# Kernel tuning notes

Measured on AMD Instinct MI355X. Metric: run time of the kernel, lower is better.

## Reference

```python
import jax, jax.numpy as jnp
import numpy as np

N = 4_000_000   # points at level d
SIDE = 1024     # coordinate range per axis
HALF = SIDE // 2  # parent coord range


def setup_inputs() -> dict:
    key = jax.random.key(0)
    k1, k2 = jax.random.split(key)
    xyz = jax.random.randint(k1, (N, 3), 0, SIDE, dtype=jnp.int32)
    b = (jnp.arange(N, dtype=jnp.int32) % 4)[:, None]  # 4 batches
    coords = jnp.concatenate([b, xyz], axis=1)          # (N,4): [b,x,y,z]
    kernel = jnp.ones((8,), dtype=jnp.float32)          # frozen all-ones 2x2x2 conv weights
    return {"coords": coords, "kernel": kernel}


def _fog(coords, kernel):
    # pos(): occupancy code 2**(x%2 + 2*y%2 + 4*z%2)
    bits = coords[:, 1:4] & 1                       # (N,3)
    off = bits[:, 0] + 2 * bits[:, 1] + 4 * bits[:, 2]  # (N,) child offset in 2x2x2 window
    pos = jnp.exp2(off.astype(jnp.float32))         # (N,) code in {1,2,4,...,128}
    contrib = pos * kernel[off]                     # per-offset conv weight (all ones)
    # stride-2 conv: parent voxel = floor(xyz/2); linearize (b,z,y,x) into a key
    parent = coords[:, 1:4] >> 1                    # (N,3)
    keys = (((coords[:, 0].astype(jnp.int64) * HALF + parent[:, 2]) * HALF
             + parent[:, 1]) * HALF + parent[:, 0])
    ukeys, inv = jnp.unique(keys, return_inverse=True, size=N, fill_value=-1)
    feats = jax.ops.segment_sum(contrib, inv, num_segments=N)[:, None]  # (N,1)
    # decode padded unique keys back to coords; pad slots -> -1
    px = (ukeys % HALF).astype(jnp.int32)
    py = ((ukeys // HALF) % HALF).astype(jnp.int32)
    pz = ((ukeys // (HALF * HALF)) % HALF).astype(jnp.int32)
    pb = (ukeys // (HALF * HALF * HALF)).astype(jnp.int32)
    valid = (ukeys >= 0)[:, None]
    coords_out = jnp.where(valid, jnp.stack([pb, px, py, pz], axis=1), -1)
    return coords_out, feats


def reference(coords, kernel):
    return _fog(coords, kernel)
```

## Files before the change

### kernel.cpp

```cpp
#include <hip/hip_runtime.h>
#include <stdint.h>

typedef unsigned int u32;
typedef unsigned long long u64;

#define LBITS  14
#define LMASK  ((1u << LBITS) - 1u)
#define NBUCK  (1u << (29 - LBITS))
#define BWORDS (1u << (LBITS - 5))
#define WPL    (BWORDS / 64)
#define WOPAD  (BWORDS + BWORDS / 32)
#define FCAP   192
#define BPB    4
#define TILE_A 4096
#define RPT    (TILE_A / 256)
#define S2     4
#define CAP2   4608
#define RPT2   (CAP2 / 256)
#define RECV   4
#define CAP    224
#define SCAN_ELEM 2048

__device__ __forceinline__ u32 woidx(u32 w) { return w + (w >> 5); }

__device__ __forceinline__ void wsync() {
    asm volatile("s_waitcnt lgkmcnt(0)" ::: "memory");
}

__device__ __forceinline__ u32 make_key(int4 c) {
    return ((((u32)c.x * 512u + ((u32)c.w >> 1)) * 512u + ((u32)c.z >> 1)) * 512u)
           + ((u32)c.y >> 1);
}

__global__ void __launch_bounds__(256) phase_a(const int4* __restrict__ coords,
        u32* __restrict__ linrec, u32* __restrict__ histmat, int n, u32 NT) {
    __shared__ u32 h[4 * 256];
    u32 t = threadIdx.x, wave = t >> 6;
    for (u32 j = t; j < 1024u; j += 256u) h[j] = 0u;
    __syncthreads();
    u32 base = blockIdx.x * TILE_A;
    u32 m = min((u32)TILE_A, (u32)n - base);
    for (u32 j = t; j < m; j += 256u) {
        int4 c = coords[base + j];
        u32 key = make_key(c);
        u32 off = ((u32)c.y & 1u) | (((u32)c.z & 1u) << 1) | (((u32)c.w & 1u) << 2);
        u32 rec = (key << 3) | off;
        linrec[base + j] = rec;
        atomicAdd(&h[wave * 256u + (rec >> 24)], 1u);
    }
    __syncthreads();
    histmat[t * NT + blockIdx.x] = h[t] + h[256u + t] + h[512u + t] + h[768u + t];
}

__global__ void scan_reduce(const u32* __restrict__ data, u32* __restrict__ partial, u32 G) {
    __shared__ u32 s[256];
    u32 t = threadIdx.x;
    u32 base = blockIdx.x * SCAN_ELEM + t * 8u;
    u32 sum = 0;
    #pragma unroll
    for (int j = 0; j < 8; ++j) { u32 idx = base + j; if (idx < G) sum += data[idx]; }
    s[t] = sum; __syncthreads();
    for (int d = 128; d > 0; d >>= 1) { if ((int)t < d) s[t] += s[t + d]; __syncthreads(); }
    if (t == 0) partial[blockIdx.x] = s[0];
}

__global__ void scan_apply2(const u32* __restrict__ data, u32* __restrict__ out,
                            const u32* __restrict__ partial, u32 G, u32 NB,
                            u32* __restrict__ total) {
    __shared__ u32 s[256];
    __shared__ u32 pb[2];
    u32 t = threadIdx.x;
    u32 p = (t < NB) ? partial[t] : 0u;
    u32 pbef = (t < blockIdx.x) ? p : 0u;
    s[t] = pbef; __syncthreads();
    for (int d = 128; d > 0; d >>= 1) { if ((int)t < d) s[t] += s[t + d]; __syncthreads(); }
    if (t == 0) pb[0] = s[0];
    __syncthreads();
    if (total) {
        s[t] = p; __syncthreads();
        for (int d = 128; d > 0; d >>= 1) { if ((int)t < d) s[t] += s[t + d]; __syncthreads(); }
        if (t == 0) pb[1] = s[0];
        __syncthreads();
        if (blockIdx.x == NB - 1u && t == 0u) total[0] = pb[1];
    }
    u32 base = blockIdx.x * SCAN_ELEM + t * 8u;
    u32 v[8]; u32 sum = 0;
    #pragma unroll
    for (int j = 0; j < 8; ++j) {
        u32 idx = base + j;
        v[j] = (idx < G) ? data[idx] : 0u;
        sum += v[j];
    }
    s[t] = sum; __syncthreads();
    for (int d = 1; d < 256; d <<= 1) {
        u32 add = (t >= (u32)d) ? s[t - d] : 0u;
        __syncthreads(); s[t] += add; __syncthreads();
    }
    u32 run = s[t] - sum + pb[0];
    #pragma unroll
    for (int j = 0; j < 8; ++j) {
        u32 idx = base + j;
        if (idx < G) { u32 x = v[j]; out[idx] = run; run += x; }
    }
}

__global__ void __launch_bounds__(256) part1(const u32* __restrict__ linrec,
        const u32* __restrict__ histmat, u32* __restrict__ tmp,
        u32* __restrict__ cursor, int n, u32 NT) {
    __shared__ u32 stage[TILE_A];
    __shared__ u32 lcur[256];
    __shared__ u32 gb[256];
    __shared__ u32 wtot[4];
    u32 t = threadIdx.x, wave = t >> 6, lane = t & 63u;
    if (blockIdx.x < 128u) cursor[blockIdx.x * 256u + t] = 0u;
    u32 base = blockIdx.x * TILE_A;
    u32 m = min((u32)TILE_A, (u32)n - base);
    u32 m4 = m >> 2, rem = m & 3u;
    lcur[t] = 0u;
    __syncthreads();
    u32 recv[RPT]; u32 tailrec = 0u;
    const uint4* lr4 = (const uint4*)(linrec + base);
    #pragma unroll
    for (int k = 0; k < RPT / 4; ++k) {
        u32 j4 = (u32)k * 256u + t;
        if (j4 < m4) {
            uint4 v = lr4[j4];
            recv[k * 4 + 0] = v.x; recv[k * 4 + 1] = v.y;
            recv[k * 4 + 2] = v.z; recv[k * 4 + 3] = v.w;
            atomicAdd(&lcur[v.x >> 24], 1u);
            atomicAdd(&lcur[v.y >> 24], 1u);
            atomicAdd(&lcur[v.z >> 24], 1u);
            atomicAdd(&lcur[v.w >> 24], 1u);
        }
    }
    if (t < rem) {
        tailrec = linrec[base + (m & ~3u) + t];
        atomicAdd(&lcur[tailrec >> 24], 1u);
    }
    __syncthreads();
    u32 v = lcur[t];
    u32 incl = v;
    #pragma unroll
    for (int d = 1; d < 64; d <<= 1) {
        u32 x = __shfl_up(incl, d);
        if ((int)lane >= d) incl += x;
    }
    if (lane == 63u) wtot[wave] = incl;
    __syncthreads();
    u32 off = (wave > 0u ? wtot[0] : 0u) + (wave > 1u ? wtot[1] : 0u)
            + (wave > 2u ? wtot[2] : 0u);
    u32 excl = off + incl - v;
    lcur[t] = excl;
    gb[t] = histmat[t * NT + blockIdx.x] - excl;
    __syncthreads();
    #pragma unroll
    for (int k = 0; k < RPT / 4; ++k) {
        u32 j4 = (u32)k * 256u + t;
        if (j4 < m4) {
            #pragma unroll
            for (int e = 0; e < 4; ++e) {
                u32 rec = recv[k * 4 + e];
                u32 pos = atomicAdd(&lcur[rec >> 24], 1u);
                stage[pos] = rec;
            }
        }
    }
    if (t < rem) {
        u32 pos = atomicAdd(&lcur[tailrec >> 24], 1u);
        stage[pos] = tailrec;
    }
    __syncthreads();
    for (u32 j = t; j < m; j += 256u) {
        u32 rec = stage[j];
        tmp[gb[rec >> 24] + j] = rec;
    }
}

__global__ void __launch_bounds__(256) part2(const u32* __restrict__ tmp,
        const u32* __restrict__ histmat, u32* __restrict__ cursor,
        u32* __restrict__ buckrec, int n, u32 NT) {
    __shared__ u32 stage[CAP2];
    __shared__ u32 lcur[128];
    __shared__ u32 dstb[128];
    __shared__ u32 wtot[2];
    u32 t = threadIdx.x, lane = t & 63u;
    u32 c = blockIdx.x / S2, s = blockIdx.x % S2;
    u32 cs = histmat[c * NT];
    u32 ce = (c == 255u) ? (u32)n : histmat[(c + 1u) * NT];
    u32 L = ce - cs;
    u32 lo = cs + L * s / S2, hi = cs + L * (s + 1u) / S2;
    u32 cnt = hi - lo;
    if (cnt <= (u32)CAP2) {
        if (t < 128u) lcur[t] = 0u;
        __syncthreads();
        u32 recv[RPT2];
        #pragma unroll
        for (int k = 0; k < RPT2; ++k) {
            u32 j = (u32)k * 256u + t;
            if (j < cnt) {
                u32 rec = tmp[lo + j];
                recv[k] = rec;
                atomicAdd(&lcur[(rec >> 17) & 127u], 1u);
            }
        }
        __syncthreads();
        u32 v = 0, incl = 0;
        if (t < 128u) {
            v = lcur[t];
            incl = v;
            #pragma unroll
            for (int d = 1; d < 64; d <<= 1) {
                u32 x = __shfl_up(incl, d);
                if ((int)lane >= d) incl += x;
            }
            if (lane == 63u) wtot[t >> 6] = incl;
        }
        __syncthreads();
        if (t < 128u) {
            u32 off = (t >= 64u) ? wtot[0] : 0u;
            u32 excl = off + incl - v;
            u32 bucket = (c << 7) | t;
            u32 gbase = atomicAdd(&cursor[bucket], v);
            lcur[t] = excl;
            dstb[t] = bucket * (u32)CAP + gbase - excl;
        }
        __syncthreads();
        #pragma unroll
        for (int k = 0; k < RPT2; ++k) {
            u32 j = (u32)k * 256u + t;
            if (j < cnt) {
                u32 rec = recv[k];
                u32 pos = atomicAdd(&lcur[(rec >> 17) & 127u], 1u);
                stage[pos] = rec;
            }
        }
        __syncthreads();
        for (u32 j = t; j < cnt; j += 256u) {
            u32 rec = stage[j];
            buckrec[dstb[(rec >> 17) & 127u] + j] = rec;
        }
    } else {
        for (u32 i = lo + t; i < hi; i += 256u) {
            u32 rec = tmp[i];
            u32 b = rec >> 17;
            u32 pos = atomicAdd(&cursor[b], 1u);
            buckrec[b * (u32)CAP + pos] = rec;
        }
    }
}

__global__ void __launch_bounds__(256) pass_count(const u32* __restrict__ buckrec,
        const u32* __restrict__ bcnt, u32* __restrict__ ucount, int n) {
    __shared__ u32 bm[BPB][WOPAD];
    u32 wave = threadIdx.x >> 6, lane = threadIdx.x & 63u;
    u32 bucket = blockIdx.x * BPB + wave;
    u32* B = bm[wave];
    #pragma unroll
    for (int j = 0; j < WPL; ++j) B[woidx(lane * WPL + j)] = 0u;
    wsync();
    u32 start = bucket * (u32)CAP;
    u32 end = start + bcnt[bucket];
    for (u32 i = start + lane; i < end; i += 64u) {
        u32 lk = (buckrec[i] >> 3) & LMASK;
        atomicOr(&B[woidx(lk >> 5)], 1u << (lk & 31u));
    }
    wsync();
    u32 sum = 0;
    #pragma unroll
    for (int j = 0; j < WPL; ++j) sum += __popc(B[woidx(lane * WPL + j)]);
    #pragma unroll
    for (int d = 1; d < 64; d <<= 1) sum += __shfl_xor(sum, d);
    if (lane == 0u) ucount[bucket] = sum;
}

__global__ void __launch_bounds__(256) pass_emit(const u32* __restrict__ buckrec,
        const u32* __restrict__ bcnt, const u32* __restrict__ ubase,
        const float* __restrict__ kern, float4* __restrict__ rows,
        float* __restrict__ feats, int n) {
    __shared__ u32 bm[BPB][WOPAD];
    __shared__ u32 wofW[BPB][BWORDS];
    __shared__ float fl[BPB][FCAP];
    __shared__ float ksc[BPB][8];
    u32 wave = threadIdx.x >> 6, lane = threadIdx.x & 63u;
    u32 bucket = blockIdx.x * BPB + wave;
    u32* B = bm[wave];
    u32* W = wofW[wave];
    float* F = fl[wave];
    #pragma unroll
    for (int j = 0; j < WPL; ++j) B[woidx(lane * WPL + j)] = 0u;
    #pragma unroll
    for (u32 j = lane; j < FCAP; j += 64u) F[j] = 0.f;
    if (lane < 8u) ksc[wave][lane] = (float)(1u << lane) * kern[lane];
    wsync();
    u32 start = bucket * (u32)CAP;
    u32 cnt = bcnt[bucket];
    u32 end = start + cnt;
    u32 recv[RECV];
    #pragma unroll
    for (int k = 0; k < RECV; ++k) {
        u32 idx = (u32)k * 64u + lane;
        if (idx < cnt) {
            u32 rec = buckrec[start + idx];
            recv[k] = rec;
            u32 lk = (rec >> 3) & LMASK;
            atomicOr(&B[woidx(lk >> 5)], 1u << (lk & 31u));
        }
    }
    wsync();
    u32 wv[WPL]; u32 pc[WPL]; u32 sum = 0;
    #pragma unroll
    for (int j = 0; j < WPL; ++j) {
        wv[j] = B[woidx(lane * WPL + j)];
        pc[j] = __popc(wv[j]);
        sum += pc[j];
    }
    u32 incl = sum;
    #pragma unroll
    for (int d = 1; d < 64; d <<= 1) {
        u32 tt = __shfl_up(incl, d);
        if ((int)lane >= d) incl += tt;
    }
    u32 lex = incl - sum;
    u32 uc = __shfl(incl, 63);
    {
        u32 r = lex;
        #pragma unroll
        for (int j = 0; j < WPL; ++j) { W[((u32)j << 6) | lane] = r; r += pc[j]; }
    }
    wsync();
    u32 base = ubase[bucket];
    bool lds_ok = (uc <= FCAP);
    if (!lds_ok) {
        for (u32 j = lane; j < uc; j += 64u) feats[base + j] = 0.f;
        asm volatile("s_waitcnt vmcnt(0)" ::: "memory");
    }
    #pragma unroll
    for (int k = 0; k < RECV; ++k) {
        u32 idx = (u32)k * 64u + lane;
        if (idx < cnt) {
            u32 rec = recv[k];
            float contrib = ksc[wave][rec & 7u];
            u32 lk = (rec >> 3) & LMASK;
            u32 w = lk >> 5, bit = lk & 31u;
            u32 r = W[((w & 7u) << 6) | (w >> 3)]
                  + __popc(B[woidx(w)] & ((1u << bit) - 1u));
            if (lds_ok) atomicAdd(&F[r], contrib);
            else        atomicAdd(&feats[base + r], contrib);
        }
    }
    wsync();
    u32 rank = base + lex;
    u32 keyhi = bucket << LBITS;
    #pragma unroll
    for (int j = 0; j < WPL; ++j) {
        u32 bits = wv[j];
        u32 kb = keyhi | ((lane * (u32)WPL + (u32)j) << 5);
        while (bits) {
            u32 tz = __builtin_ctz(bits);
            bits &= bits - 1u;
            u32 key = kb | tz;
            rows[rank++] = make_float4((float)(key >> 27), (float)(key & 511u),
                                       (float)((key >> 9) & 511u),
                                       (float)((key >> 18) & 511u));
        }
    }
    if (lds_ok) {
        for (u32 j = lane; j < uc; j += 64u) feats[base + j] = F[j];
    }
}

__global__ void pad_fill(float4* __restrict__ rows, float* __restrict__ feats,
                         const u32* __restrict__ counter, int n) {
    int i = blockIdx.x * blockDim.x + threadIdx.x;
    if (i < n && (u32)i >= counter[0]) {
        rows[i] = make_float4(-1.f, -1.f, -1.f, -1.f);
        feats[i] = 0.f;
    }
}

extern "C" void kernel_launch(void* const* d_in, const int* in_sizes, int n_in,
                              void* d_out, int out_size, void* d_ws, size_t ws_size,
                              hipStream_t stream) {
    const int n = in_sizes[0] / 4;
    const int4* coords = (const int4*)d_in[0];
    const float* kern  = (const float*)d_in[1];
    const u32 NT = ((u32)n + TILE_A - 1) / TILE_A;
    const u32 G1 = 256 * NT;
    const u32 NB1 = (G1 + SCAN_ELEM - 1) / SCAN_ELEM;
    const u32 NB3 = (NBUCK + SCAN_ELEM - 1) / SCAN_ELEM;

    u32* wsp = (u32*)d_ws;
    u32* tmp     = wsp;
    u32* histmat = tmp + n;
    u32* cursor  = histmat + G1;
    u32* ucount  = cursor + NBUCK;
    u32* counter = ucount + NBUCK;
    u32* spart   = counter + 4;
    u32* linrec  = spart + 256;
    u32* buckrec = linrec;

    float4* rows  = (float4*)d_out;
    float*  feats = (float*)((char*)d_out + (size_t)n * 16);

    phase_a<<<NT, 256, 0, stream>>>(coords, linrec, histmat, n, NT);
    scan_reduce<<<NB1, 256, 0, stream>>>(histmat, spart, G1);
    scan_apply2<<<NB1, 256, 0, stream>>>(histmat, histmat, spart, G1, NB1, (u32*)nullptr);
    part1<<<NT, 256, 0, stream>>>(linrec, histmat, tmp, cursor, n, NT);
    part2<<<256 * S2, 256, 0, stream>>>(tmp, histmat, cursor, buckrec, n, NT);
    pass_count<<<NBUCK / BPB, 256, 0, stream>>>(buckrec, cursor, ucount, n);
    scan_reduce<<<NB3, 256, 0, stream>>>(ucount, spart, NBUCK);
    scan_apply2<<<NB3, 256, 0, stream>>>(ucount, ucount, spart, NBUCK, NB3, counter);
    pass_emit<<<NBUCK / BPB, 256, 0, stream>>>(buckrec, cursor, ucount, kern,
                                               rows, feats, n);
    pad_fill<<<((u32)n + 255) / 256, 256, 0, stream>>>(rows, feats, counter, n);
}
```

Measured before the change: 220.5 us.

## Fuse two-pass scans into single-kernel scan and double radix tile size

Replaces the reduce-then-apply scan pair with a single kernel in which each block recomputes the sum of all preceding elements by itself. This removes two kernel launches and the partial-sum buffer, at the cost of redundant prefix reads that grow with the block index. The scan output now goes to separate buffers (histex, ubase), so the inputs are no longer overwritten in place. The radix partition tile grows from 4096 to 8192 and the part2 split from 4 to 2, halving the block counts while doubling LDS staging per block.

```diff
diff --git a/kernel.cpp b/kernel.cpp
--- a/kernel.cpp
+++ b/kernel.cpp
@@ -12,10 +12,10 @@
 #define WOPAD  (BWORDS + BWORDS / 32)
 #define FCAP   192
 #define BPB    4
-#define TILE_A 4096
+#define TILE_A 8192
 #define RPT    (TILE_A / 256)
-#define S2     4
-#define CAP2   4608
+#define S2     2
+#define CAP2   9216
 #define RPT2   (CAP2 / 256)
 #define RECV   4
 #define CAP    224
@@ -52,38 +52,19 @@
     histmat[t * NT + blockIdx.x] = h[t] + h[256u + t] + h[512u + t] + h[768u + t];
 }
 
-__global__ void scan_reduce(const u32* __restrict__ data, u32* __restrict__ partial, u32 G) {
+__global__ void scan_one(const u32* __restrict__ data, u32* __restrict__ out,
+                         u32 G, u32 NB, u32* __restrict__ total) {
     __shared__ u32 s[256];
+    __shared__ u32 pb;
     u32 t = threadIdx.x;
-    u32 base = blockIdx.x * SCAN_ELEM + t * 8u;
-    u32 sum = 0;
-    #pragma unroll
-    for (int j = 0; j < 8; ++j) { u32 idx = base + j; if (idx < G) sum += data[idx]; }
-    s[t] = sum; __syncthreads();
+    u32 pred = blockIdx.x * SCAN_ELEM;
+    u32 sum0 = 0;
+    for (u32 i = t; i < pred; i += 256u) sum0 += data[i];
+    s[t] = sum0; __syncthreads();
     for (int d = 128; d > 0; d >>= 1) { if ((int)t < d) s[t] += s[t + d]; __syncthreads(); }
-    if (t == 0) partial[blockIdx.x] = s[0];
-}
-
-__global__ void scan_apply2(const u32* __restrict__ data, u32* __restrict__ out,
-                            const u32* __restrict__ partial, u32 G, u32 NB,
-                            u32* __restrict__ total) {
-    __shared__ u32 s[256];
-    __shared__ u32 pb[2];
-    u32 t = threadIdx.x;
-    u32 p = (t < NB) ? partial[t] : 0u;
-    u32 pbef = (t < blockIdx.x) ? p : 0u;
-    s[t] = pbef; __syncthreads();
-    for (int d = 128; d > 0; d >>= 1) { if ((int)t < d) s[t] += s[t + d]; __syncthreads(); }
-    if (t == 0) pb[0] = s[0];
-    __syncthreads();
-    if (total) {
-        s[t] = p; __syncthreads();
-        for (int d = 128; d > 0; d >>= 1) { if ((int)t < d) s[t] += s[t + d]; __syncthreads(); }
-        if (t == 0) pb[1] = s[0];
-        __syncthreads();
-        if (blockIdx.x == NB - 1u && t == 0u) total[0] = pb[1];
-    }
-    u32 base = blockIdx.x * SCAN_ELEM + t * 8u;
+    if (t == 0) pb = s[0];
+    __syncthreads();
+    u32 base = pred + t * 8u;
     u32 v[8]; u32 sum = 0;
     #pragma unroll
     for (int j = 0; j < 8; ++j) {
@@ -96,16 +77,17 @@
         u32 add = (t >= (u32)d) ? s[t - d] : 0u;
         __syncthreads(); s[t] += add; __syncthreads();
     }
-    u32 run = s[t] - sum + pb[0];
+    u32 run = s[t] - sum + pb;
     #pragma unroll
     for (int j = 0; j < 8; ++j) {
         u32 idx = base + j;
         if (idx < G) { u32 x = v[j]; out[idx] = run; run += x; }
     }
+    if (total && blockIdx.x == NB - 1u && t == 255u) total[0] = pb + s[255];
 }
 
 __global__ void __launch_bounds__(256) part1(const u32* __restrict__ linrec,
-        const u32* __restrict__ histmat, u32* __restrict__ tmp,
+        const u32* __restrict__ histex, u32* __restrict__ tmp,
         u32* __restrict__ cursor, int n, u32 NT) {
     __shared__ u32 stage[TILE_A];
     __shared__ u32 lcur[256];
@@ -151,7 +133,7 @@
             + (wave > 2u ? wtot[2] : 0u);
     u32 excl = off + incl - v;
     lcur[t] = excl;
-    gb[t] = histmat[t * NT + blockIdx.x] - excl;
+    gb[t] = histex[t * NT + blockIdx.x] - excl;
     __syncthreads();
     #pragma unroll
     for (int k = 0; k < RPT / 4; ++k) {
@@ -177,7 +159,7 @@
 }
 
 __global__ void __launch_bounds__(256) part2(const u32* __restrict__ tmp,
-        const u32* __restrict__ histmat, u32* __restrict__ cursor,
+        const u32* __restrict__ histex, u32* __restrict__ cursor,
         u32* __restrict__ buckrec, int n, u32 NT) {
     __shared__ u32 stage[CAP2];
     __shared__ u32 lcur[128];
@@ -185,8 +167,8 @@
     __shared__ u32 wtot[2];
     u32 t = threadIdx.x, lane = t & 63u;
     u32 c = blockIdx.x / S2, s = blockIdx.x % S2;
-    u32 cs = histmat[c * NT];
-    u32 ce = (c == 255u) ? (u32)n : histmat[(c + 1u) * NT];
+    u32 cs = histex[c * NT];
+    u32 ce = (c == 255u) ? (u32)n : histex[(c + 1u) * NT];
     u32 L = ce - cs;
     u32 lo = cs + L * s / S2, hi = cs + L * (s + 1u) / S2;
     u32 cnt = hi - lo;
@@ -294,7 +276,6 @@
     wsync();
     u32 start = bucket * (u32)CAP;
     u32 cnt = bcnt[bucket];
-    u32 end = start + cnt;
     u32 recv[RECV];
     #pragma unroll
     for (int k = 0; k < RECV; ++k) {
@@ -392,25 +373,24 @@
     u32* wsp = (u32*)d_ws;
     u32* tmp     = wsp;
     u32* histmat = tmp + n;
-    u32* cursor  = histmat + G1;
+    u32* histex  = histmat + G1;
+    u32* cursor  = histex + G1;
     u32* ucount  = cursor + NBUCK;
-    u32* counter = ucount + NBUCK;
-    u32* spart   = counter + 4;
-    u32* linrec  = spart + 256;
+    u32* ubase   = ucount + NBUCK;
+    u32* counter = ubase + NBUCK;
+    u32* linrec  = counter + 4;
     u32* buckrec = linrec;
 
     float4* rows  = (float4*)d_out;
     float*  feats = (float*)((char*)d_out + (size_t)n * 16);
 
     phase_a<<<NT, 256, 0, stream>>>(coords, linrec, histmat, n, NT);
-    scan_reduce<<<NB1, 256, 0, stream>>>(histmat, spart, G1);
-    scan_apply2<<<NB1, 256, 0, stream>>>(histmat, histmat, spart, G1, NB1, (u32*)nullptr);
-    part1<<<NT, 256, 0, stream>>>(linrec, histmat, tmp, cursor, n, NT);
-    part2<<<256 * S2, 256, 0, stream>>>(tmp, histmat, cursor, buckrec, n, NT);
+    scan_one<<<NB1, 256, 0, stream>>>(histmat, histex, G1, NB1, (u32*)nullptr);
+    part1<<<NT, 256, 0, stream>>>(linrec, histex, tmp, cursor, n, NT);
+    part2<<<256 * S2, 256, 0, stream>>>(tmp, histex, cursor, buckrec, n, NT);
     pass_count<<<NBUCK / BPB, 256, 0, stream>>>(buckrec, cursor, ucount, n);
-    scan_reduce<<<NB3, 256, 0, stream>>>(ucount, spart, NBUCK);
-    scan_apply2<<<NB3, 256, 0, stream>>>(ucount, ucount, spart, NBUCK, NB3, counter);
-    pass_emit<<<NBUCK / BPB, 256, 0, stream>>>(buckrec, cursor, ucount, kern,
+    scan_one<<<NB3, 256, 0, stream>>>(ucount, ubase, NBUCK, NB3, counter);
+    pass_emit<<<NBUCK / BPB, 256, 0, stream>>>(buckrec, cursor, ubase, kern,
                                                rows, feats, n);
     pad_fill<<<((u32)n + 255) / 256, 256, 0, stream>>>(rows, feats, counter, n);
 }
```

Measured after the change: 297.6 us. 35.0% more time.
